# Performance work log

Measured on AMD Instinct MI355X. Metric: run time of the kernel, lower is better.

The kernel has to match this reference:

```python
import jax, jax.numpy as jnp
import numpy as np

B_, N, C, H = 8192, 49, 192, 6
HD = C // H
SCALE = HD ** -0.5


def setup_inputs() -> dict:
    key = jax.random.key(0)
    k0, k1, k2, k3 = jax.random.split(key, 4)
    x = jax.random.normal(k0, (B_, N, C), dtype=jnp.float32)
    mask = jax.random.randint(k1, (B_, N), 0, 2, dtype=jnp.int32)
    w_qkv = jax.random.normal(k2, (C, 3 * C), dtype=jnp.float32) * 0.02
    b_qkv = jnp.zeros((3 * C,), dtype=jnp.float32)
    w_proj = jax.random.normal(k3, (C, C), dtype=jnp.float32) * 0.02
    b_proj = jnp.zeros((C,), dtype=jnp.float32)
    return {"x": x, "mask": mask, "w_qkv": w_qkv, "b_qkv": b_qkv,
            "w_proj": w_proj, "b_proj": b_proj}


def reference(x, mask, w_qkv, b_qkv, w_proj, b_proj):
    # qkv projection: [B_, N, 3C] -> [3, B_, H, N, HD]
    qkv = (x @ w_qkv + b_qkv).reshape(B_, N, 3, H, HD).transpose(2, 0, 3, 1, 4)
    q, k, v = qkv[0], qkv[1], qkv[2]
    # scaled QK^T: [B_, H, N, N]
    attn = jnp.einsum('bhnd,bhmd->bhnm', q, k) * SCALE
    # additive key mask: mask==0 positions get -inf
    attn = jnp.where(mask[:, None, None, :] == 0, -jnp.inf, attn)
    p = jax.nn.softmax(attn, axis=-1)  # dropout p=0 -> identity
    out = jnp.einsum('bhnm,bhmd->bhnd', p, v)  # AV
    out = out.transpose(0, 2, 1, 3).reshape(B_, N, C)
    return out @ w_proj + b_proj
```

## Files before the change

### kernel.cpp

```cpp
#include <hip/hip_runtime.h>


typedef __attribute__((ext_vector_type(8))) short short8;
typedef __attribute__((ext_vector_type(4))) float f32x4;

#define SCALE 0.17677669529663687f

__device__ __forceinline__ unsigned short f2bf(float x) {
    union { float f; unsigned int i; } v; v.f = x;
    return (unsigned short)((v.i + 0x7FFFu + ((v.i >> 16) & 1u)) >> 16);
}

__device__ __forceinline__ int swz32(int row, int col) {
    return row * 32 + ((((col >> 3) ^ (row & 3)) << 3) | (col & 7));
}
__device__ __forceinline__ int swz64(int row, int col) {
    return row * 64 + ((((col >> 3) ^ (row & 7)) << 3) | (col & 7));
}

__global__ void repack_kernel(const float* __restrict__ wqkv,
                              const float* __restrict__ wproj,
                              unsigned short* __restrict__ wq_pack,
                              unsigned short* __restrict__ wp_pack) {
    int idx = blockIdx.x * 256 + threadIdx.x;
    if (idx < 6 * 576 * 32) {
        int kk  = idx & 31;
        int col = (idx >> 5) % 576;
        int kt  = idx / (576 * 32);
        wq_pack[idx] = f2bf(wqkv[(kt * 32 + kk) * 576 + col]);
    } else {
        int j = idx - 6 * 576 * 32;
        if (j < 6 * 192 * 32) {
            int kk  = j & 31;
            int col = (j >> 5) % 192;
            int kt  = j / (192 * 32);
            wp_pack[j] = f2bf(wproj[(kt * 32 + kk) * 192 + col]);
        }
    }
}

__global__ __launch_bounds__(384, 3)
void win_attn_kernel(const float* __restrict__ x,
                     const int* __restrict__ mask,
                     const float* __restrict__ bqkv,
                     const float* __restrict__ bproj,
                     const unsigned short* __restrict__ wq,
                     const unsigned short* __restrict__ wpj,
                     float* __restrict__ out) {
    __shared__ __align__(16) unsigned short region[36864];
    __shared__ float mbias[64];

    const int b    = blockIdx.x;
    const int tid  = threadIdx.x;
    const int lane = tid & 63;
    const int h    = tid >> 6;
    const int quad = lane >> 4;
    const int l16  = lane & 15;

    const float* xb = x + (size_t)b * 9408;
    for (int i4 = tid; i4 < 2352; i4 += 384) {
        int flat = i4 * 4;
        int n = flat / 192, c = flat % 192;
        float4 v = *(const float4*)(const void*)&xb[flat];
        ushort4 pk = make_ushort4(f2bf(v.x), f2bf(v.y), f2bf(v.z), f2bf(v.w));
        *(ushort4*)(void*)&region[n * 200 + c] = pk;
    }
    if (tid < 375) {
        uint4 z = {0u, 0u, 0u, 0u};
        *(uint4*)(void*)&region[9800 + tid * 8] = z;
    }
    if (tid < 64)
        mbias[tid] = (tid < 49 && mask[b * 49 + tid] != 0) ? 0.0f : -1e30f;
    __syncthreads();

    f32x4 acc[6][4];
    #pragma unroll
    for (int t = 0; t < 6; ++t)
        #pragma unroll
        for (int mt = 0; mt < 4; ++mt)
            acc[t][mt] = (f32x4){0.f, 0.f, 0.f, 0.f};

    int colb[6];
    #pragma unroll
    for (int t = 0; t < 6; ++t) colb[t] = (t >> 1) * 192 + h * 32 + (t & 1) * 16;

    #pragma unroll
    for (int kt = 0; kt < 6; ++kt) {
        short8 af[4];
        #pragma unroll
        for (int mt = 0; mt < 4; ++mt)
            af[mt] = *(const short8*)(const void*)
                     &region[(mt * 16 + l16) * 200 + kt * 32 + quad * 8];
        #pragma unroll
        for (int t = 0; t < 6; ++t) {
            short8 bw = *(const short8*)(const void*)
                        &wq[(size_t)(kt * 576 + colb[t] + l16) * 32 + quad * 8];
            #pragma unroll
            for (int mt = 0; mt < 4; ++mt)
                acc[t][mt] = __builtin_amdgcn_mfma_f32_16x16x32_bf16(
                                 af[mt], bw, acc[t][mt], 0, 0, 0);
        }
    }
    #pragma unroll
    for (int t = 0; t < 6; ++t) {
        float bv = bqkv[colb[t] + l16];
        #pragma unroll
        for (int mt = 0; mt < 4; ++mt)
            #pragma unroll
            for (int r = 0; r < 4; ++r)
                acc[t][mt][r] += bv;
    }
    __syncthreads();

    unsigned short* qb  = &region[h * 6144];
    unsigned short* kb  = qb + 2048;
    unsigned short* vtb = qb + 4096;
    #pragma unroll
    for (int t = 0; t < 2; ++t)
        #pragma unroll
        for (int mt = 0; mt < 4; ++mt)
            #pragma unroll
            for (int r = 0; r < 4; ++r) {
                int row = mt * 16 + quad * 4 + r;
                qb[swz32(row, t * 16 + l16)] = f2bf(acc[t    ][mt][r]);
                kb[swz32(row, t * 16 + l16)] = f2bf(acc[t + 2][mt][r]);
            }
    #pragma unroll
    for (int t = 0; t < 2; ++t)
        #pragma unroll
        for (int mt = 0; mt < 4; ++mt) {
            int d = t * 16 + l16;
            ushort4 pk = make_ushort4(f2bf(acc[4 + t][mt][0]), f2bf(acc[4 + t][mt][1]),
                                      f2bf(acc[4 + t][mt][2]), f2bf(acc[4 + t][mt][3]));
            *(ushort4*)(void*)&vtb[swz64(d, mt * 16 + quad * 4)] = pk;
        }

    f32x4 s[4][4];
    #pragma unroll
    for (int mt = 0; mt < 4; ++mt)
        #pragma unroll
        for (int nt = 0; nt < 4; ++nt)
            s[mt][nt] = (f32x4){0.f, 0.f, 0.f, 0.f};

    {
        short8 aq[4], bk[4];
        #pragma unroll
        for (int mt = 0; mt < 4; ++mt)
            aq[mt] = *(const short8*)(const void*)&qb[swz32(mt * 16 + l16, quad * 8)];
        #pragma unroll
        for (int nt = 0; nt < 4; ++nt)
            bk[nt] = *(const short8*)(const void*)&kb[swz32(nt * 16 + l16, quad * 8)];
        #pragma unroll
        for (int mt = 0; mt < 4; ++mt)
            #pragma unroll
            for (int nt = 0; nt < 4; ++nt)
                s[mt][nt] = __builtin_amdgcn_mfma_f32_16x16x32_bf16(
                                aq[mt], bk[nt], s[mt][nt], 0, 0, 0);
    }

    float mb[4];
    #pragma unroll
    for (int nt = 0; nt < 4; ++nt) mb[nt] = mbias[nt * 16 + l16];

    #pragma unroll
    for (int mt = 0; mt < 4; ++mt) {
        #pragma unroll
        for (int r = 0; r < 4; ++r) {
            float v0 = s[mt][0][r] * SCALE + mb[0];
            float v1 = s[mt][1][r] * SCALE + mb[1];
            float v2 = s[mt][2][r] * SCALE + mb[2];
            float v3 = s[mt][3][r] * SCALE + mb[3];
            float mx = fmaxf(fmaxf(v0, v1), fmaxf(v2, v3));
            mx = fmaxf(mx, __shfl_xor(mx, 1));
            mx = fmaxf(mx, __shfl_xor(mx, 2));
            mx = fmaxf(mx, __shfl_xor(mx, 4));
            mx = fmaxf(mx, __shfl_xor(mx, 8));
            float e0 = __expf(v0 - mx), e1 = __expf(v1 - mx);
            float e2 = __expf(v2 - mx), e3 = __expf(v3 - mx);
            float sum = e0 + e1 + e2 + e3;
            sum += __shfl_xor(sum, 1);
            sum += __shfl_xor(sum, 2);
            sum += __shfl_xor(sum, 4);
            sum += __shfl_xor(sum, 8);
            float inv = 1.0f / sum;
            s[mt][0][r] = e0 * inv; s[mt][1][r] = e1 * inv;
            s[mt][2][r] = e2 * inv; s[mt][3][r] = e3 * inv;
        }
    }

    unsigned short* pb = qb;
    #pragma unroll
    for (int mt = 0; mt < 4; ++mt)
        #pragma unroll
        for (int nt = 0; nt < 4; ++nt)
            #pragma unroll
            for (int r = 0; r < 4; ++r)
                pb[swz64(mt * 16 + quad * 4 + r, nt * 16 + l16)] = f2bf(s[mt][nt][r]);

    f32x4 o[4][2];
    #pragma unroll
    for (int mt = 0; mt < 4; ++mt)
        #pragma unroll
        for (int dt = 0; dt < 2; ++dt)
            o[mt][dt] = (f32x4){0.f, 0.f, 0.f, 0.f};

    #pragma unroll
    for (int kt = 0; kt < 2; ++kt) {
        short8 ap[4], bv[2];
        #pragma unroll
        for (int mt = 0; mt < 4; ++mt)
            ap[mt] = *(const short8*)(const void*)
                     &pb[swz64(mt * 16 + l16, kt * 32 + quad * 8)];
        #pragma unroll
        for (int dt = 0; dt < 2; ++dt)
            bv[dt] = *(const short8*)(const void*)
                     &vtb[swz64(dt * 16 + l16, kt * 32 + quad * 8)];
        #pragma unroll
        for (int mt = 0; mt < 4; ++mt)
            #pragma unroll
            for (int dt = 0; dt < 2; ++dt)
                o[mt][dt] = __builtin_amdgcn_mfma_f32_16x16x32_bf16(
                                ap[mt], bv[dt], o[mt][dt], 0, 0, 0);
    }

    __syncthreads();
    #pragma unroll
    for (int dt = 0; dt < 2; ++dt)
        #pragma unroll
        for (int mt = 0; mt < 4; ++mt)
            #pragma unroll
            for (int r = 0; r < 4; ++r)
                region[(mt * 16 + quad * 4 + r) * 200 + h * 32 + dt * 16 + l16]
                    = f2bf(o[mt][dt][r]);
    __syncthreads();

    f32x4 po[2][4];
    #pragma unroll
    for (int nt = 0; nt < 2; ++nt)
        #pragma unroll
        for (int mt = 0; mt < 4; ++mt)
            po[nt][mt] = (f32x4){0.f, 0.f, 0.f, 0.f};

    #pragma unroll
    for (int kt = 0; kt < 6; ++kt) {
        short8 ao[4];
        #pragma unroll
        for (int mt = 0; mt < 4; ++mt)
            ao[mt] = *(const short8*)(const void*)
                     &region[(mt * 16 + l16) * 200 + kt * 32 + quad * 8];
        #pragma unroll
        for (int nt = 0; nt < 2; ++nt) {
            int col = h * 32 + nt * 16 + l16;
            short8 bw = *(const short8*)(const void*)
                        &wpj[(size_t)(kt * 192 + col) * 32 + quad * 8];
            #pragma unroll
            for (int mt = 0; mt < 4; ++mt)
                po[nt][mt] = __builtin_amdgcn_mfma_f32_16x16x32_bf16(
                                 ao[mt], bw, po[nt][mt], 0, 0, 0);
        }
    }

    #pragma unroll
    for (int nt = 0; nt < 2; ++nt) {
        int col = h * 32 + nt * 16 + l16;
        float bv = bproj[col];
        #pragma unroll
        for (int mt = 0; mt < 4; ++mt)
            #pragma unroll
            for (int r = 0; r < 4; ++r) {
                int row = mt * 16 + quad * 4 + r;
                if (row < 49)
                    out[(size_t)b * 9408 + row * 192 + col] = po[nt][mt][r] + bv;
            }
    }
}

extern "C" void kernel_launch(void* const* d_in, const int* in_sizes, int n_in,
                              void* d_out, int out_size, void* d_ws, size_t ws_size,
                              hipStream_t stream) {
    const float* x      = (const float*)d_in[0];
    const int*   mask   = (const int*)d_in[1];
    const float* w_qkv  = (const float*)d_in[2];
    const float* b_qkv  = (const float*)d_in[3];
    const float* w_proj = (const float*)d_in[4];
    const float* b_proj = (const float*)d_in[5];
    float*       out    = (float*)d_out;

    unsigned short* wq_pack = (unsigned short*)d_ws;
    unsigned short* wp_pack = wq_pack + 110592;

    repack_kernel<<<(110592 + 36864 + 255) / 256, 256, 0, stream>>>(
        w_qkv, w_proj, wq_pack, wp_pack);
    win_attn_kernel<<<8192, 384, 0, stream>>>(x, mask, b_qkv, b_proj,
                                              wq_pack, wp_pack, out);
}
```

Before: 993.7 us.

## Keep Q/K/P in registers via cross-lane shuffle transposes instead of LDS round-trips

Computes Q and K projections transposed (swapping MFMA operands) so their accumulators can be repacked into MFMA input fragments with lane shuffles, removing the LDS stores and loads of Q, K and P. The scores are computed as S^T, so softmax reduces across lanes 16/32 apart, and P is transposed into A-fragments with shuffles. It also adds packed bf16 conversion via v_cvt_pk_bf16_f32, shrinks shared memory, and drops the min-blocks launch bound. The trade is extra shuffle and register traffic, and possibly higher register pressure affecting occupancy, in exchange for less LDS traffic and no post-QKV sync.

```diff
diff --git a/kernel.cpp b/kernel.cpp
--- a/kernel.cpp
+++ b/kernel.cpp
@@ -11,11 +11,35 @@
     return (unsigned short)((v.i + 0x7FFFu + ((v.i >> 16) & 1u)) >> 16);
 }
 
-__device__ __forceinline__ int swz32(int row, int col) {
-    return row * 32 + ((((col >> 3) ^ (row & 3)) << 3) | (col & 7));
-}
+__device__ __forceinline__ unsigned int pkbf(float lo, float hi) {
+    unsigned int r;
+    asm("v_cvt_pk_bf16_f32 %0, %1, %2" : "=v"(r) : "v"(lo), "v"(hi));
+    return r;
+}
+
 __device__ __forceinline__ int swz64(int row, int col) {
     return row * 64 + ((((col >> 3) ^ (row & 7)) << 3) | (col & 7));
+}
+
+__device__ __forceinline__ short8 xpose(f32x4 tlo, f32x4 thi, int srcA, bool hi) {
+    unsigned int pl0 = pkbf(tlo[0], tlo[1]);
+    unsigned int pl1 = pkbf(tlo[2], tlo[3]);
+    unsigned int ph0 = pkbf(thi[0], thi[1]);
+    unsigned int ph1 = pkbf(thi[2], thi[3]);
+    unsigned int a0 = (unsigned int)__shfl((int)pl0, srcA);
+    unsigned int b0 = (unsigned int)__shfl((int)ph0, srcA);
+    unsigned int a1 = (unsigned int)__shfl((int)pl1, srcA);
+    unsigned int b1 = (unsigned int)__shfl((int)ph1, srcA);
+    unsigned int a2 = (unsigned int)__shfl((int)pl0, srcA + 16);
+    unsigned int b2 = (unsigned int)__shfl((int)ph0, srcA + 16);
+    unsigned int a3 = (unsigned int)__shfl((int)pl1, srcA + 16);
+    unsigned int b3 = (unsigned int)__shfl((int)ph1, srcA + 16);
+    union { short8 s8; unsigned int u[4]; } f;
+    f.u[0] = hi ? b0 : a0;
+    f.u[1] = hi ? b1 : a1;
+    f.u[2] = hi ? b2 : a2;
+    f.u[3] = hi ? b3 : a3;
+    return f.s8;
 }
 
 __global__ void repack_kernel(const float* __restrict__ wqkv,
@@ -39,7 +63,7 @@
     }
 }
 
-__global__ __launch_bounds__(384, 3)
+__global__ __launch_bounds__(384)
 void win_attn_kernel(const float* __restrict__ x,
                      const int* __restrict__ mask,
                      const float* __restrict__ bqkv,
@@ -47,8 +71,8 @@
                      const unsigned short* __restrict__ wq,
                      const unsigned short* __restrict__ wpj,
                      float* __restrict__ out) {
-    __shared__ __align__(16) unsigned short region[36864];
-    __shared__ float mbias[64];
+    __shared__ __align__(16) unsigned short region[25088];
+    __shared__ __align__(16) float mbias[64];
 
     const int b    = blockIdx.x;
     const int tid  = threadIdx.x;
@@ -62,8 +86,10 @@
         int flat = i4 * 4;
         int n = flat / 192, c = flat % 192;
         float4 v = *(const float4*)(const void*)&xb[flat];
-        ushort4 pk = make_ushort4(f2bf(v.x), f2bf(v.y), f2bf(v.z), f2bf(v.w));
-        *(ushort4*)(void*)&region[n * 200 + c] = pk;
+        uint2 pk;
+        pk.x = pkbf(v.x, v.y);
+        pk.y = pkbf(v.z, v.w);
+        *(uint2*)(void*)&region[n * 200 + c] = pk;
     }
     if (tid < 375) {
         uint4 z = {0u, 0u, 0u, 0u};
@@ -96,13 +122,27 @@
             short8 bw = *(const short8*)(const void*)
                         &wq[(size_t)(kt * 576 + colb[t] + l16) * 32 + quad * 8];
             #pragma unroll
-            for (int mt = 0; mt < 4; ++mt)
-                acc[t][mt] = __builtin_amdgcn_mfma_f32_16x16x32_bf16(
-                                 af[mt], bw, acc[t][mt], 0, 0, 0);
-        }
-    }
-    #pragma unroll
-    for (int t = 0; t < 6; ++t) {
+            for (int mt = 0; mt < 4; ++mt) {
+                if (t < 4)
+                    acc[t][mt] = __builtin_amdgcn_mfma_f32_16x16x32_bf16(
+                                     bw, af[mt], acc[t][mt], 0, 0, 0);
+                else
+                    acc[t][mt] = __builtin_amdgcn_mfma_f32_16x16x32_bf16(
+                                     af[mt], bw, acc[t][mt], 0, 0, 0);
+            }
+        }
+    }
+    #pragma unroll
+    for (int t = 0; t < 4; ++t) {
+        f32x4 bq = *(const f32x4*)(const void*)&bqkv[colb[t] + quad * 4];
+        #pragma unroll
+        for (int nt = 0; nt < 4; ++nt)
+            #pragma unroll
+            for (int r = 0; r < 4; ++r)
+                acc[t][nt][r] += bq[r];
+    }
+    #pragma unroll
+    for (int t = 4; t < 6; ++t) {
         float bv = bqkv[colb[t] + l16];
         #pragma unroll
         for (int mt = 0; mt < 4; ++mt)
@@ -110,30 +150,28 @@
             for (int r = 0; r < 4; ++r)
                 acc[t][mt][r] += bv;
     }
-    __syncthreads();
-
-    unsigned short* qb  = &region[h * 6144];
-    unsigned short* kb  = qb + 2048;
-    unsigned short* vtb = qb + 4096;
-    #pragma unroll
-    for (int t = 0; t < 2; ++t)
-        #pragma unroll
-        for (int mt = 0; mt < 4; ++mt)
-            #pragma unroll
-            for (int r = 0; r < 4; ++r) {
-                int row = mt * 16 + quad * 4 + r;
-                qb[swz32(row, t * 16 + l16)] = f2bf(acc[t    ][mt][r]);
-                kb[swz32(row, t * 16 + l16)] = f2bf(acc[t + 2][mt][r]);
-            }
+
+    unsigned short* vtb = &region[12800 + h * 2048];
     #pragma unroll
     for (int t = 0; t < 2; ++t)
         #pragma unroll
         for (int mt = 0; mt < 4; ++mt) {
             int d = t * 16 + l16;
-            ushort4 pk = make_ushort4(f2bf(acc[4 + t][mt][0]), f2bf(acc[4 + t][mt][1]),
-                                      f2bf(acc[4 + t][mt][2]), f2bf(acc[4 + t][mt][3]));
-            *(ushort4*)(void*)&vtb[swz64(d, mt * 16 + quad * 4)] = pk;
-        }
+            uint2 pk;
+            pk.x = pkbf(acc[4 + t][mt][0], acc[4 + t][mt][1]);
+            pk.y = pkbf(acc[4 + t][mt][2], acc[4 + t][mt][3]);
+            *(uint2*)(void*)&vtb[swz64(d, mt * 16 + quad * 4)] = pk;
+        }
+
+    const int  srcA = ((lane & 16) << 1) | l16;
+    const bool hiq  = (lane & 32) != 0;
+
+    short8 qf[4], kf[4];
+    #pragma unroll
+    for (int nt = 0; nt < 4; ++nt) {
+        qf[nt] = xpose(acc[0][nt], acc[1][nt], srcA, hiq);
+        kf[nt] = xpose(acc[2][nt], acc[3][nt], srcA, hiq);
+    }
 
     f32x4 s[4][4];
     #pragma unroll
@@ -141,86 +179,79 @@
         #pragma unroll
         for (int nt = 0; nt < 4; ++nt)
             s[mt][nt] = (f32x4){0.f, 0.f, 0.f, 0.f};
-
-    {
-        short8 aq[4], bk[4];
-        #pragma unroll
-        for (int mt = 0; mt < 4; ++mt)
-            aq[mt] = *(const short8*)(const void*)&qb[swz32(mt * 16 + l16, quad * 8)];
+    #pragma unroll
+    for (int mt = 0; mt < 4; ++mt)
         #pragma unroll
         for (int nt = 0; nt < 4; ++nt)
-            bk[nt] = *(const short8*)(const void*)&kb[swz32(nt * 16 + l16, quad * 8)];
-        #pragma unroll
-        for (int mt = 0; mt < 4; ++mt)
-            #pragma unroll
-            for (int nt = 0; nt < 4; ++nt)
-                s[mt][nt] = __builtin_amdgcn_mfma_f32_16x16x32_bf16(
-                                aq[mt], bk[nt], s[mt][nt], 0, 0, 0);
-    }
-
-    float mb[4];
-    #pragma unroll
-    for (int nt = 0; nt < 4; ++nt) mb[nt] = mbias[nt * 16 + l16];
-
-    #pragma unroll
-    for (int mt = 0; mt < 4; ++mt) {
-        #pragma unroll
-        for (int r = 0; r < 4; ++r) {
-            float v0 = s[mt][0][r] * SCALE + mb[0];
-            float v1 = s[mt][1][r] * SCALE + mb[1];
-            float v2 = s[mt][2][r] * SCALE + mb[2];
-            float v3 = s[mt][3][r] * SCALE + mb[3];
-            float mx = fmaxf(fmaxf(v0, v1), fmaxf(v2, v3));
-            mx = fmaxf(mx, __shfl_xor(mx, 1));
-            mx = fmaxf(mx, __shfl_xor(mx, 2));
-            mx = fmaxf(mx, __shfl_xor(mx, 4));
-            mx = fmaxf(mx, __shfl_xor(mx, 8));
-            float e0 = __expf(v0 - mx), e1 = __expf(v1 - mx);
-            float e2 = __expf(v2 - mx), e3 = __expf(v3 - mx);
-            float sum = e0 + e1 + e2 + e3;
-            sum += __shfl_xor(sum, 1);
-            sum += __shfl_xor(sum, 2);
-            sum += __shfl_xor(sum, 4);
-            sum += __shfl_xor(sum, 8);
-            float inv = 1.0f / sum;
-            s[mt][0][r] = e0 * inv; s[mt][1][r] = e1 * inv;
-            s[mt][2][r] = e2 * inv; s[mt][3][r] = e3 * inv;
-        }
-    }
-
-    unsigned short* pb = qb;
+            s[mt][nt] = __builtin_amdgcn_mfma_f32_16x16x32_bf16(
+                            kf[mt], qf[nt], s[mt][nt], 0, 0, 0);
+
+    f32x4 mb4[4];
     #pragma unroll
     for (int mt = 0; mt < 4; ++mt)
-        #pragma unroll
-        for (int nt = 0; nt < 4; ++nt)
-            #pragma unroll
-            for (int r = 0; r < 4; ++r)
-                pb[swz64(mt * 16 + quad * 4 + r, nt * 16 + l16)] = f2bf(s[mt][nt][r]);
+        mb4[mt] = *(const f32x4*)(const void*)&mbias[mt * 16 + quad * 4];
+
+    #pragma unroll
+    for (int nt = 0; nt < 4; ++nt) {
+        float ev[4][4];
+        float pm[4];
+        #pragma unroll
+        for (int mt = 0; mt < 4; ++mt) {
+            #pragma unroll
+            for (int r = 0; r < 4; ++r)
+                ev[mt][r] = s[mt][nt][r] * SCALE + mb4[mt][r];
+            pm[mt] = fmaxf(fmaxf(ev[mt][0], ev[mt][1]),
+                           fmaxf(ev[mt][2], ev[mt][3]));
+        }
+        float mx = fmaxf(fmaxf(pm[0], pm[1]), fmaxf(pm[2], pm[3]));
+        mx = fmaxf(mx, __shfl_xor(mx, 16));
+        mx = fmaxf(mx, __shfl_xor(mx, 32));
+        float ps[4];
+        #pragma unroll
+        for (int mt = 0; mt < 4; ++mt) {
+            #pragma unroll
+            for (int r = 0; r < 4; ++r)
+                ev[mt][r] = __expf(ev[mt][r] - mx);
+            ps[mt] = (ev[mt][0] + ev[mt][1]) + (ev[mt][2] + ev[mt][3]);
+        }
+        float sum = (ps[0] + ps[1]) + (ps[2] + ps[3]);
+        sum += __shfl_xor(sum, 16);
+        sum += __shfl_xor(sum, 32);
+        float inv = 1.0f / sum;
+        #pragma unroll
+        for (int mt = 0; mt < 4; ++mt)
+            #pragma unroll
+            for (int r = 0; r < 4; ++r)
+                s[mt][nt][r] = ev[mt][r] * inv;
+    }
+
+    short8 ap[4][2];
+    #pragma unroll
+    for (int mo = 0; mo < 4; ++mo)
+        #pragma unroll
+        for (int kt = 0; kt < 2; ++kt)
+            ap[mo][kt] = xpose(s[kt * 2][mo], s[kt * 2 + 1][mo], srcA, hiq);
 
     f32x4 o[4][2];
     #pragma unroll
-    for (int mt = 0; mt < 4; ++mt)
+    for (int mo = 0; mo < 4; ++mo)
         #pragma unroll
         for (int dt = 0; dt < 2; ++dt)
-            o[mt][dt] = (f32x4){0.f, 0.f, 0.f, 0.f};
+            o[mo][dt] = (f32x4){0.f, 0.f, 0.f, 0.f};
 
     #pragma unroll
     for (int kt = 0; kt < 2; ++kt) {
-        short8 ap[4], bv[2];
-        #pragma unroll
-        for (int mt = 0; mt < 4; ++mt)
-            ap[mt] = *(const short8*)(const void*)
-                     &pb[swz64(mt * 16 + l16, kt * 32 + quad * 8)];
+        short8 bvv[2];
         #pragma unroll
         for (int dt = 0; dt < 2; ++dt)
-            bv[dt] = *(const short8*)(const void*)
-                     &vtb[swz64(dt * 16 + l16, kt * 32 + quad * 8)];
-        #pragma unroll
-        for (int mt = 0; mt < 4; ++mt)
+            bvv[dt] = *(const short8*)(const void*)
+                      &vtb[swz64(dt * 16 + l16, kt * 32 + quad * 8)];
+        #pragma unroll
+        for (int mo = 0; mo < 4; ++mo)
             #pragma unroll
             for (int dt = 0; dt < 2; ++dt)
-                o[mt][dt] = __builtin_amdgcn_mfma_f32_16x16x32_bf16(
-                                ap[mt], bv[dt], o[mt][dt], 0, 0, 0);
+                o[mo][dt] = __builtin_amdgcn_mfma_f32_16x16x32_bf16(
+                                ap[mo][kt], bvv[dt], o[mo][dt], 0, 0, 0);
     }
 
     __syncthreads();
```

Result: faster. 850.4 us (-14.4%).
